# Kernel optimization log

Hardware: AMD Instinct MI355X
Metric: run time of the kernel (lower is better)

## Reference

```python
import jax, jax.numpy as jnp
import numpy as np

N0, N1 = 4096, 16384
HID, LAT, DIM, OUT = 128, 64, 3, 3
OFFS = [1, 2, 3, 5, 8]  # circulant graph offsets; A+A^3 support is offset sums


def _ring_edges(N, offs):
    # edge_index of A + A^3 for circulant adjacency with given offsets
    o = np.asarray(offs)
    s3 = (o[:, None, None] + o[None, :, None] + o[None, None, :]).ravel()
    aug = np.unique(np.concatenate([o, s3]))
    src = np.repeat(np.arange(N), aug.size)
    dst = (src + np.tile(aug, N)) % N
    return np.stack([src, dst]).astype(np.int32)


def _gatv2(x, src, dst, eattr, Wl, bl, Wr, br, We, att, bias, N):
    # PyG GATv2Conv, heads=1, add_self_loops=True with fill_value='mean'
    cnt = jax.ops.segment_sum(jnp.ones_like(dst, jnp.float32), dst, N)
    loop_attr = jax.ops.segment_sum(eattr, dst, N) / jnp.maximum(cnt, 1.0)[:, None]
    loops = jnp.arange(N, dtype=src.dtype)
    s = jnp.concatenate([src, loops])
    d = jnp.concatenate([dst, loops])
    ea = jnp.concatenate([eattr, loop_attr], 0)
    xl = x @ Wl.T + bl
    xr = x @ Wr.T + br
    m = xl[s] + xr[d] + ea @ We.T              # [E+N, HID]
    m = jnp.where(m > 0, m, 0.2 * m)           # leaky_relu(0.2)
    a = m @ att                                # [E+N]
    amax = jax.ops.segment_max(a, d, N)
    ex = jnp.exp(a - amax[d])
    den = jax.ops.segment_sum(ex, d, N)
    alpha = ex / (den[d] + 1e-16)
    return jax.ops.segment_sum(xl[s] * alpha[:, None], d, N) + bias


def _knn_interp(x, pos_x, pos_y, k=3):
    # PyG knn_interpolate: inverse-squared-distance weighted k-NN average
    d2 = (jnp.sum(pos_y ** 2, 1)[:, None] + jnp.sum(pos_x ** 2, 1)[None, :]
          - 2.0 * pos_y @ pos_x.T)             # [Ny, Nx]
    neg, idx = jax.lax.top_k(-d2, k)
    w = 1.0 / jnp.maximum(-neg, 1e-16)          # [Ny, k]
    return jnp.sum(x[idx] * w[..., None], 1) / jnp.sum(w, 1)[:, None]


def _forward(latent, pos0, pos1, eidx0, eidx1, conv_Wl, conv_bl, conv_Wr,
             conv_br, conv_We, conv_att, conv_bias, lin0_W, lin0_b, lins_W,
             lins_b, out_W, out_b):
    x = latent @ lin0_W.T + lin0_b
    src0, dst0 = eidx0[0], eidx0[1]
    ea0 = pos0[dst0] - pos0[src0]
    for c in (0, 1):
        h = jnp.concatenate([x, pos0], 1)
        x = jax.nn.elu(_gatv2(h, src0, dst0, ea0, conv_Wl[c], conv_bl[c],
                              conv_Wr[c], conv_br[c], conv_We[c], conv_att[c],
                              conv_bias[c], N0)) + h @ lins_W[c].T + lins_b[c]
    x = _knn_interp(x, pos0, pos1, 3)
    src1, dst1 = eidx1[0], eidx1[1]
    ea1 = pos1[dst1] - pos1[src1]
    for c in (2, 3):
        h = jnp.concatenate([x, pos1], 1)
        x = jax.nn.elu(_gatv2(h, src1, dst1, ea1, conv_Wl[c], conv_bl[c],
                              conv_Wr[c], conv_br[c], conv_We[c], conv_att[c],
                              conv_bias[c], N1)) + h @ lins_W[c].T + lins_b[c]
    h = jnp.concatenate([x, pos1], 1)
    return h @ out_W.T + out_b


def setup_inputs() -> dict:
    key = jax.random.key(0)
    ks = jax.random.split(key, 16)
    n = lambda i, shape, s=0.05: jax.random.normal(ks[i], shape, jnp.float32) * s
    IN = HID + DIM
    return dict(
        latent=jax.random.normal(ks[0], (N0, LAT), jnp.float32),
        pos0=jax.random.normal(ks[1], (N0, DIM), jnp.float32),
        pos1=jax.random.normal(ks[2], (N1, DIM), jnp.float32),
        eidx0=jnp.asarray(_ring_edges(N0, OFFS)),
        eidx1=jnp.asarray(_ring_edges(N1, OFFS)),
        conv_Wl=n(3, (4, HID, IN)), conv_bl=n(4, (4, HID)),
        conv_Wr=n(5, (4, HID, IN)), conv_br=n(6, (4, HID)),
        conv_We=n(7, (4, HID, DIM)), conv_att=n(8, (4, HID)),
        conv_bias=n(9, (4, HID)),
        lin0_W=n(10, (HID, LAT)), lin0_b=n(11, (HID,)),
        lins_W=n(12, (4, HID, IN)), lins_b=n(13, (4, HID)),
        out_W=n(14, (OUT, IN)), out_b=n(15, (OUT,)))


def reference(latent, pos0, pos1, eidx0, eidx1, conv_Wl, conv_bl, conv_Wr,
              conv_br, conv_We, conv_att, conv_bias, lin0_W, lin0_b, lins_W,
              lins_b, out_W, out_b):
    return _forward(latent, pos0, pos1, eidx0, eidx1, conv_Wl, conv_bl,
                    conv_Wr, conv_br, conv_We, conv_att, conv_bias, lin0_W,
                    lin0_b, lins_W, lins_b, out_W, out_b)
```

## Files before the change

### kernel.cpp

```cpp
#include <hip/hip_runtime.h>
#include <hip/hip_bf16.h>

#define N0 4096
#define N1 16384
#define HID 128
#define LAT 64
#define DIM 3
#define NAUG 21
#define JTOT 512
#define NG 5

typedef __attribute__((ext_vector_type(8))) short bf16x8;
typedef __attribute__((ext_vector_type(4))) float f32x4;

__device__ __constant__ int c_aug[NAUG] = {1,2,3,4,5,6,7,8,9,10,11,12,13,14,
                                           15,16,17,18,19,21,24};

__device__ __forceinline__ unsigned short f2bf(float v) {
    __hip_bfloat16 b = __float2bfloat16(v);
    return *reinterpret_cast<unsigned short*>(&b);
}

template<int CTRL>
__device__ __forceinline__ float dpp_xadd(float p) {
    return p + __int_as_float(__builtin_amdgcn_mov_dpp(
        __float_as_int(p), CTRL, 0xF, 0xF, true));
}

__device__ __forceinline__ float reduce32(float p) {
    p = dpp_xadd<0xB1>(p);
    p = dpp_xadd<0x4E>(p);
    p = dpp_xadd<0x128>(p);
    p += __shfl_xor(p, 4, 64);
    p += __shfl_xor(p, 16, 64);
    return p;
}

#define KCH 16
#define KCS 256
#define KNN_XPARTS 64
#define KNN_BLOCKS (KCH * KNN_XPARTS)

#define WSWZ_PER_LAYER 81920
#define H0G4 131072
#define H1G4 524288
#define P_NSWZ (4 * WSWZ_PER_LAYER)
#define P_B0 P_NSWZ
#define P_B1 (P_B0 + 4 * JTOT)
#define P_B2 (P_B1 + 64 * 128)
#define P_B3 (P_B2 + H0G4)
#define P_B4 (P_B3 + H1G4)
#define PREP_BLOCKS 3880

__global__ __launch_bounds__(256)
void prep_knn_kernel(const float* __restrict__ Wl,
                     const float* __restrict__ Wr,
                     const float* __restrict__ We,
                     const float* __restrict__ linsW,
                     const float* __restrict__ bl,
                     const float* __restrict__ br,
                     const float* __restrict__ linsb,
                     const float* __restrict__ lin0W,
                     const float* __restrict__ pos0,
                     const float* __restrict__ pos1,
                     unsigned short* __restrict__ Wswz,
                     float* __restrict__ bias_cat,
                     float* __restrict__ Wt0,
                     unsigned short* __restrict__ hswz0A,
                     unsigned short* __restrict__ hswz0B,
                     unsigned short* __restrict__ hswz1A,
                     unsigned short* __restrict__ hswz1B,
                     float* __restrict__ pb_d,
                     int* __restrict__ pb_i) {
    __shared__ float4 sx[KCS];

    if (blockIdx.x < KNN_BLOCKS) {
        int tid = threadIdx.x;
        int chunk = blockIdx.x >> 6;
        int xpart = blockIdx.x & 63;
        {
            const float* p = &pos0[(chunk * KCS + tid) * 3];
            float x = p[0], y = p[1], z = p[2];
            sx[tid] = make_float4(x, y, z, x * x + y * y + z * z);
        }
        __syncthreads();
        int y = xpart * 256 + tid;
        float p0 = pos1[y * 3], p1 = pos1[y * 3 + 1], p2 = pos1[y * 3 + 2];
        float m0 = -2.0f * p0, m1 = -2.0f * p1, m2 = -2.0f * p2;
        float sy = p0 * p0 + p1 * p1 + p2 * p2;
        float bd0 = 1e30f, bd1 = 1e30f, bd2 = 1e30f;
        int bi0 = 0, bi1 = 0, bi2 = 0;
        int gbase = chunk * KCS;
#pragma unroll 4
        for (int i = 0; i < KCS; i += 4) {
            float4 s[4];
#pragma unroll
            for (int v = 0; v < 4; ++v) s[v] = sx[i + v];
#pragma unroll
            for (int v = 0; v < 4; ++v) {
                int gi = gbase + i + v;
                float t = fmaf(m0, s[v].x, s[v].w);
                t = fmaf(m1, s[v].y, t);
                t = fmaf(m2, s[v].z, t);
                t += sy;
                bool c0 = t < bd0;
                bool c1 = t < bd1;
                bool c2 = t < bd2;
                float n0 = fminf(bd0, t);
                float n1 = __builtin_amdgcn_fmed3f(bd0, bd1, t);
                float n2 = __builtin_amdgcn_fmed3f(bd1, bd2, t);
                int j0 = c0 ? gi : bi0;
                int j1 = c0 ? bi0 : (c1 ? gi : bi1);
                int j2 = c1 ? bi1 : (c2 ? gi : bi2);
                bd0 = n0; bd1 = n1; bd2 = n2;
                bi0 = j0; bi1 = j1; bi2 = j2;
            }
        }
        int base = (chunk * N1 + y) * 3;
        pb_d[base] = bd0; pb_d[base + 1] = bd1; pb_d[base + 2] = bd2;
        pb_i[base] = bi0; pb_i[base + 1] = bi1; pb_i[base + 2] = bi2;
        return;
    }

    int tid = (blockIdx.x - KNN_BLOCKS) * blockDim.x + threadIdx.x;
    if (tid < P_NSWZ) {
        int c = tid / WSWZ_PER_LAYER;
        int r = tid - c * WSWZ_PER_LAYER;
        int nt = r / 2560;
        int g  = (r / 512) % 5;
        int l  = (r / 8) % 64;
        int j  = r % 8;
        int k  = g * 32 + (l >> 4) * 8 + j;
        int n  = nt * 16 + (l & 15);
        float v = 0.0f;
        if (k < 131) {
            if (n < 128)      v = Wl[(c * 128 + n) * 131 + k];
            else if (n < 256) v = Wr[(c * 128 + (n - 128)) * 131 + k];
            else if (n < 384) v = linsW[(c * 128 + (n - 256)) * 131 + k];
            else              v = (k >= 128) ? We[(c * 128 + (n - 384)) * 3 + (k - 128)]
                                             : 0.0f;
        }
        Wswz[tid] = f2bf(v);
    } else if (tid < P_B1) {
        int idx = tid - P_B0;
        int c = idx / JTOT;
        int j = idx - c * JTOT;
        float v;
        if (j < 128)        v = bl[c * 128 + j];
        else if (j < 256)   v = br[c * 128 + (j - 128)];
        else if (j < 384)   v = linsb[c * 128 + (j - 256)];
        else                v = 0.0f;
        bias_cat[idx] = v;
    } else if (tid < P_B2) {
        int idx = tid - P_B1;
        int k = idx / 128;
        int j = idx - k * 128;
        Wt0[idx] = lin0W[j * 64 + k];
    } else if (tid < P_B3) {
        int r = tid - P_B2;
        int j = r & 7;
        int l = (r >> 3) & 63;
        int mt = r >> 9;
        int row = mt * 16 + (l & 15);
        int k = 128 + (l >> 4) * 8 + j;
        float v = (k < 131) ? pos0[row * 3 + (k - 128)] : 0.0f;
        unsigned short bv = f2bf(v);
        size_t idx = (size_t)((mt * 5 + 4) * 64 + l) * 8 + j;
        hswz0A[idx] = bv;
        hswz0B[idx] = bv;
    } else if (tid < P_B4) {
        int r = tid - P_B3;
        int j = r & 7;
        int l = (r >> 3) & 63;
        int mt = r >> 9;
        int row = mt * 16 + (l & 15);
        int k = 128 + (l >> 4) * 8 + j;
        float v = (k < 131) ? pos1[row * 3 + (k - 128)] : 0.0f;
        unsigned short bv = f2bf(v);
        size_t idx = (size_t)((mt * 5 + 4) * 64 + l) * 8 + j;
        hswz1A[idx] = bv;
        hswz1B[idx] = bv;
    }
}

#define MERGE_BLOCKS 128

__global__ __launch_bounds__(128)
void lin0_merge_kernel(const float* __restrict__ latent,
                       const float* __restrict__ Wt0,
                       const float* __restrict__ b,
                       unsigned short* __restrict__ hswz0,
                       const float* __restrict__ pb_d,
                       const int* __restrict__ pb_i,
                       int* __restrict__ knn_idx,
                       float* __restrict__ knn_w) {
    __shared__ float lrow[64];

    if (blockIdx.x < MERGE_BLOCKS) {
        int y = blockIdx.x * 128 + threadIdx.x;
        float bd0 = 1e30f, bd1 = 1e30f, bd2 = 1e30f;
        int bi0 = 0, bi1 = 0, bi2 = 0;
        for (int c = 0; c < KCH; ++c) {
            int base = (c * N1 + y) * 3;
#pragma unroll
            for (int t3 = 0; t3 < 3; ++t3) {
                float t = pb_d[base + t3];
                int gi = pb_i[base + t3];
                bool c0 = t < bd0;
                bool c1 = t < bd1;
                bool c2 = t < bd2;
                float n0 = fminf(bd0, t);
                float n1 = __builtin_amdgcn_fmed3f(bd0, bd1, t);
                float n2 = __builtin_amdgcn_fmed3f(bd1, bd2, t);
                int j0 = c0 ? gi : bi0;
                int j1 = c0 ? bi0 : (c1 ? gi : bi1);
                int j2 = c1 ? bi1 : (c2 ? gi : bi2);
                bd0 = n0; bd1 = n1; bd2 = n2;
                bi0 = j0; bi1 = j1; bi2 = j2;
            }
        }
        knn_idx[y * 3]     = bi0;
        knn_idx[y * 3 + 1] = bi1;
        knn_idx[y * 3 + 2] = bi2;
        knn_w[y * 3]     = 1.0f / fmaxf(bd0, 1e-16f);
        knn_w[y * 3 + 1] = 1.0f / fmaxf(bd1, 1e-16f);
        knn_w[y * 3 + 2] = 1.0f / fmaxf(bd2, 1e-16f);
        return;
    }

    int n = blockIdx.x - MERGE_BLOCKS;
    int j = threadIdx.x;
    if (j < 64) lrow[j] = latent[n * 64 + j];
    __syncthreads();
    float acc = b[j];
#pragma unroll 8
    for (int k = 0; k < 64; ++k) acc += lrow[k] * Wt0[k * 128 + j];
    int g = j >> 5, sub = (j >> 3) & 3, jj = j & 7;
    hswz0[(size_t)(((n >> 4) * 5 + g) * 64 + sub * 16 + (n & 15)) * 8 + jj] = f2bf(acc);
}

#define WROW 40
#define FSTR 132

__device__ __forceinline__ void layer_body(
        const unsigned short* __restrict__ hswz,
        const unsigned short* __restrict__ Wswz,
        const float* __restrict__ bias_cat,
        const float* __restrict__ att,
        const float* __restrict__ bias,
        float* __restrict__ xout,
        unsigned short* __restrict__ hout,
        const float* __restrict__ outW,
        const float* __restrict__ outb,
        const float* __restrict__ pos1,
        int mode, int N, int mt0,
        float (*xls_s)[FSTR], float (*pes_s)[FSTR], float (*xr_s)[FSTR],
        float (*lin_s)[FSTR]) {
    int tid = threadIdx.x;
    int w = tid >> 6;
    int l = tid & 63;
    int quad = l >> 4, lcol = l & 15;
    int n0 = mt0 * 16;
    int MT = N >> 4;

    bf16x8 a[3][NG];
#pragma unroll
    for (int i = 0; i < 3; ++i) {
        int mt = mt0 - 2 + i;
        if (mt < 0) mt += MT;
#pragma unroll
        for (int g = 0; g < NG; ++g)
            a[i][g] = *(const bf16x8*)&hswz[(size_t)((mt * NG + g) * 64 + l) * 8];
    }

#pragma unroll
    for (int i = 0; i < 4; ++i) {
        int b = i * 8 + w;
        int colbase = (b & 7) * 16;
        int ntw, kind;
        if (b < 8)       { ntw = b;      kind = 0; }
        else if (b < 16) { ntw = 16 + b; kind = 1; }
        else if (b < 24) { ntw = b - 8;  kind = 2; }
        else             { ntw = b - 8;  kind = 3; }
        bf16x8 bf[NG];
#pragma unroll
        for (int g = 0; g < NG; ++g)
            bf[g] = *(const bf16x8*)&Wswz[(size_t)((ntw * NG + g) * 64 + l) * 8];
        float bv = bias_cat[ntw * 16 + lcol];
        if (kind < 2) {
            float (*dst)[FSTR] = (kind == 0) ? xls_s : pes_s;
#pragma unroll
            for (int m = 0; m < 3; ++m) {
                f32x4 c = {bv, bv, bv, bv};
#pragma unroll
                for (int g = 0; g < NG; ++g)
                    c = __builtin_amdgcn_mfma_f32_16x16x32_bf16(a[m][g], bf[g], c, 0, 0, 0);
                if (m == 0) {
                    if (quad >= 2) {
                        int w0 = (quad - 2) * 4;
#pragma unroll
                        for (int r = 0; r < 4; ++r) dst[w0 + r][colbase + lcol] = c[r];
                    }
                } else {
                    int w0 = m * 16 - 8 + quad * 4;
#pragma unroll
                    for (int r = 0; r < 4; ++r) dst[w0 + r][colbase + lcol] = c[r];
                }
            }
        } else {
            f32x4 c = {bv, bv, bv, bv};
#pragma unroll
            for (int g = 0; g < NG; ++g)
                c = __builtin_amdgcn_mfma_f32_16x16x32_bf16(a[2][g], bf[g], c, 0, 0, 0);
            float (*dst)[FSTR] = (kind == 2) ? xr_s : lin_s;
            int w0 = quad * 4;
#pragma unroll
            for (int r = 0; r < 4; ++r) dst[w0 + r][colbase + lcol] = c[r];
        }
    }
    __syncthreads();

    int qh = l >> 5;
    int t = l & 31;
    int dl = w * 2 + qh;
    int d = n0 + dl;
    int selfrow = dl + 24;
    int i0 = t * 4;

    f32x4 linv = *(const f32x4*)&lin_s[dl][i0];

    float att4[4], base[4], xld[4], pesum[4], o[4];
    {
        f32x4 a0 = *(const f32x4*)&att[i0];
        f32x4 r0 = *(const f32x4*)&xr_s[dl][i0];
        f32x4 x0 = *(const f32x4*)&xls_s[selfrow][i0];
        f32x4 p0 = *(const f32x4*)&pes_s[selfrow][i0];
#pragma unroll
        for (int j = 0; j < 4; ++j) {
            att4[j] = a0[j];
            xld[j]  = x0[j];
            base[j] = r0[j] + p0[j];
            pesum[j] = 0.0f;
            o[j] = 0.0f;
        }
    }

    float den = 0.0f;

#pragma unroll
    for (int k = 0; k < NAUG; ++k) {
        int lr = selfrow - c_aug[k];
        float xls[4], pes[4];
        *(f32x4*)&xls[0] = *(const f32x4*)&xls_s[lr][i0];
        *(f32x4*)&pes[0] = *(const f32x4*)&pes_s[lr][i0];
        float p = 0.0f;
#pragma unroll
        for (int j = 0; j < 4; ++j) {
            float mm = xls[j] + base[j] - pes[j];
            mm = mm > 0.0f ? mm : 0.2f * mm;
            p = fmaf(att4[j], mm, p);
            pesum[j] += pes[j];
        }
        p = reduce32(p);
        float wgt = __expf(p);
        den += wgt;
#pragma unroll
        for (int j = 0; j < 4; ++j) o[j] = fmaf(wgt, xls[j], o[j]);
    }
    {
        const float inv21 = 1.0f / 21.0f;
        float p = 0.0f;
#pragma unroll
        for (int j = 0; j < 4; ++j) {
            float mm = xld[j] + base[j] - pesum[j] * inv21;
            mm = mm > 0.0f ? mm : 0.2f * mm;
            p = fmaf(att4[j], mm, p);
        }
        p = reduce32(p);
        float wgt = __expf(p);
        den += wgt;
#pragma unroll
        for (int j = 0; j < 4; ++j) o[j] = fmaf(wgt, xld[j], o[j]);
    }

    float inv = 1.0f / (den + 1e-16f);
    float res[4];
    {
        f32x4 b0 = *(const f32x4*)&bias[i0];
#pragma unroll
        for (int j = 0; j < 4; ++j) {
            float v = o[j] * inv + b0[j];
            v = v > 0.0f ? v : __expf(v) - 1.0f;
            res[j] = v + linv[j];
        }
    }

    if (mode == 0) {
        *(f32x4*)&xout[(size_t)d * 128 + i0] = *(f32x4*)&res[0];
    } else if (mode == 1) {
        unsigned short ob[4];
#pragma unroll
        for (int j = 0; j < 4; ++j) ob[j] = f2bf(res[j]);
        int g = i0 >> 5, sub = (i0 >> 3) & 3, jj = i0 & 7;
        *(uint2*)&hout[(size_t)((((d >> 4) * 5 + g) * 64) + sub * 16 + (d & 15)) * 8 + jj]
            = *(uint2*)ob;
    } else {
        float po[3];
#pragma unroll
        for (int o3 = 0; o3 < 3; ++o3) {
            const float* wr = &outW[o3 * 131 + i0];
            float p = res[0] * wr[0];
            p = fmaf(res[1], wr[1], p);
            p = fmaf(res[2], wr[2], p);
            p = fmaf(res[3], wr[3], p);
            p = reduce32(p);
            po[o3] = p;
        }
        if (t == 0) {
            float p0 = pos1[d * 3], p1 = pos1[d * 3 + 1], p2 = pos1[d * 3 + 2];
#pragma unroll
            for (int o3 = 0; o3 < 3; ++o3) {
                xout[d * 3 + o3] = po[o3] + outb[o3] + p0 * outW[o3 * 131 + 128]
                                 + p1 * outW[o3 * 131 + 129] + p2 * outW[o3 * 131 + 130];
            }
        }
    }
}

__global__ __launch_bounds__(512, 2)
void fused_layer_kernel(const unsigned short* __restrict__ hswz,
                        const unsigned short* __restrict__ Wswz,
                        const float* __restrict__ bias_cat,
                        const float* __restrict__ att,
                        const float* __restrict__ bias,
                        float* __restrict__ xout,
                        unsigned short* __restrict__ hout,
                        const float* __restrict__ outW,
                        const float* __restrict__ outb,
                        const float* __restrict__ pos1,
                        int mode, int N) {
    __shared__ __align__(16) float xls_s[WROW][FSTR];
    __shared__ __align__(16) float pes_s[WROW][FSTR];
    __shared__ __align__(16) float xr_s[16][FSTR];
    __shared__ __align__(16) float lin_s[16][FSTR];
    layer_body(hswz, Wswz, bias_cat, att, bias, xout, hout,
               outW, outb, pos1, mode, N, blockIdx.x,
               xls_s, pes_s, xr_s, lin_s);
}

__global__ __launch_bounds__(256)
void interp_kernel(const float* __restrict__ x0, const int* __restrict__ knn_idx,
                   const float* __restrict__ knn_w, unsigned short* __restrict__ hswz) {
    int wave = threadIdx.x >> 6;
    int lane = threadIdx.x & 63;
    int y = blockIdx.x * 4 + wave;
    int i0 = 2 * lane;
    float w0 = knn_w[y * 3], w1 = knn_w[y * 3 + 1], w2 = knn_w[y * 3 + 2];
    int j0 = knn_idx[y * 3], j1 = knn_idx[y * 3 + 1], j2 = knn_idx[y * 3 + 2];
    float inv = 1.0f / (w0 + w1 + w2);
    float2 a = *(const float2*)&x0[(size_t)j0 * 128 + i0];
    float2 b = *(const float2*)&x0[(size_t)j1 * 128 + i0];
    float2 c = *(const float2*)&x0[(size_t)j2 * 128 + i0];
    float rx = (w0 * a.x + w1 * b.x + w2 * c.x) * inv;
    float ry = (w0 * a.y + w1 * b.y + w2 * c.y) * inv;
    unsigned int packed = (unsigned int)f2bf(rx) | ((unsigned int)f2bf(ry) << 16);
    int g = i0 >> 5, sub = (i0 >> 3) & 3, jj = i0 & 7;
    size_t idx = (size_t)((((y >> 4) * 5 + g) * 64) + sub * 16 + (y & 15)) * 8 + jj;
    *(unsigned int*)&hswz[idx] = packed;
}

extern "C" void kernel_launch(void* const* d_in, const int* in_sizes, int n_in,
                              void* d_out, int out_size, void* d_ws, size_t ws_size,
                              hipStream_t stream) {
    (void)in_sizes; (void)n_in; (void)out_size; (void)ws_size;
    const float* latent   = (const float*)d_in[0];
    const float* pos0     = (const float*)d_in[1];
    const float* pos1     = (const float*)d_in[2];
    const float* conv_Wl  = (const float*)d_in[5];
    const float* conv_bl  = (const float*)d_in[6];
    const float* conv_Wr  = (const float*)d_in[7];
    const float* conv_br  = (const float*)d_in[8];
    const float* conv_We  = (const float*)d_in[9];
    const float* conv_att = (const float*)d_in[10];
    const float* conv_bias= (const float*)d_in[11];
    const float* lin0_W   = (const float*)d_in[12];
    const float* lin0_b   = (const float*)d_in[13];
    const float* lins_W   = (const float*)d_in[14];
    const float* lins_b   = (const float*)d_in[15];
    const float* out_W    = (const float*)d_in[16];
    const float* out_b    = (const float*)d_in[17];
    float* out = (float*)d_out;

    char* ws = (char*)d_ws;
    unsigned short* Wswz = (unsigned short*)ws; ws += (size_t)4 * WSWZ_PER_LAYER * 2;
    float* bias_cat = (float*)ws;  ws += (size_t)4 * JTOT * 4;
    float* Wt0      = (float*)ws;  ws += (size_t)64 * 128 * 4;
    unsigned short* hswz0A = (unsigned short*)ws; ws += (size_t)(N0 / 16) * NG * 64 * 8 * 2;
    unsigned short* hswz0B = (unsigned short*)ws; ws += (size_t)(N0 / 16) * NG * 64 * 8 * 2;
    unsigned short* hswz1A = (unsigned short*)ws; ws += (size_t)(N1 / 16) * NG * 64 * 8 * 2;
    unsigned short* hswz1B = (unsigned short*)ws; ws += (size_t)(N1 / 16) * NG * 64 * 8 * 2;
    float* bufA     = (float*)ws;  ws += (size_t)N0 * 128 * 4;
    float* pb_d     = (float*)ws;  ws += (size_t)KCH * N1 * 3 * 4;
    int*   pb_i     = (int*)ws;    ws += (size_t)KCH * N1 * 3 * 4;
    int*   knn_idx  = (int*)ws;    ws += (size_t)N1 * 3 * 4;
    float* knn_w    = (float*)ws;  ws += (size_t)N1 * 3 * 4;

    prep_knn_kernel<<<KNN_BLOCKS + PREP_BLOCKS, 256, 0, stream>>>(
        conv_Wl, conv_Wr, conv_We, lins_W, conv_bl, conv_br, lins_b, lin0_W,
        pos0, pos1, Wswz, bias_cat, Wt0, hswz0A, hswz0B, hswz1A, hswz1B,
        pb_d, pb_i);

    lin0_merge_kernel<<<MERGE_BLOCKS + N0, 128, 0, stream>>>(
        latent, Wt0, lin0_b, hswz0A, pb_d, pb_i, knn_idx, knn_w);

    fused_layer_kernel<<<N0 / 16, 512, 0, stream>>>(
        hswz0A, Wswz + (size_t)0 * WSWZ_PER_LAYER, bias_cat + 0 * JTOT,
        conv_att + 0 * 128, conv_bias + 0 * 128, nullptr, hswz0B,
        nullptr, nullptr, nullptr, 1, N0);
    fused_layer_kernel<<<N0 / 16, 512, 0, stream>>>(
        hswz0B, Wswz + (size_t)1 * WSWZ_PER_LAYER, bias_cat + 1 * JTOT,
        conv_att + 1 * 128, conv_bias + 1 * 128, bufA, nullptr,
        nullptr, nullptr, nullptr, 0, N0);

    interp_kernel<<<N1 / 4, 256, 0, stream>>>(bufA, knn_idx, knn_w, hswz1A);

    fused_layer_kernel<<<N1 / 16, 512, 0, stream>>>(
        hswz1A, Wswz + (size_t)2 * WSWZ_PER_LAYER, bias_cat + 2 * JTOT,
        conv_att + 2 * 128, conv_bias + 2 * 128, nullptr, hswz1B,
        nullptr, nullptr, nullptr, 1, N1);
    fused_layer_kernel<<<N1 / 16, 512, 0, stream>>>(
        hswz1B, Wswz + (size_t)3 * WSWZ_PER_LAYER, bias_cat + 3 * JTOT,
        conv_att + 3 * 128, conv_bias + 3 * 128, out, nullptr,
        out_W, out_b, pos1, 2, N1);
}
```

Before: 203.1 us.

## Fuse kNN interpolation into first fine-level GAT layer kernel

Removes the separate interp kernel and its global hswz1A buffer. Each fine-level layer block now computes the interpolated features, plus the pos columns for its 3 halo tiles, straight into shared memory and reads its A fragments from there. This drops one launch and one global round trip, but each tile's interpolation is recomputed three times across neighbouring blocks. The change also replaces one shuffle-xor step in the reduction with a DPP row-shift add.

```diff
diff --git a/kernel.cpp b/kernel.cpp
--- a/kernel.cpp
+++ b/kernel.cpp
@@ -31,7 +31,7 @@
     p = dpp_xadd<0xB1>(p);
     p = dpp_xadd<0x4E>(p);
     p = dpp_xadd<0x128>(p);
-    p += __shfl_xor(p, 4, 64);
+    p = dpp_xadd<0x124>(p);
     p += __shfl_xor(p, 16, 64);
     return p;
 }
@@ -68,7 +68,6 @@
                      float* __restrict__ Wt0,
                      unsigned short* __restrict__ hswz0A,
                      unsigned short* __restrict__ hswz0B,
-                     unsigned short* __restrict__ hswz1A,
                      unsigned short* __restrict__ hswz1B,
                      float* __restrict__ pb_d,
                      int* __restrict__ pb_i) {
@@ -176,10 +175,7 @@
         int row = mt * 16 + (l & 15);
         int k = 128 + (l >> 4) * 8 + j;
         float v = (k < 131) ? pos1[row * 3 + (k - 128)] : 0.0f;
-        unsigned short bv = f2bf(v);
-        size_t idx = (size_t)((mt * 5 + 4) * 64 + l) * 8 + j;
-        hswz1A[idx] = bv;
-        hswz1B[idx] = bv;
+        hswz1B[(size_t)((mt * 5 + 4) * 64 + l) * 8 + j] = f2bf(v);
     }
 }
 
@@ -244,6 +240,7 @@
 
 __device__ __forceinline__ void layer_body(
         const unsigned short* __restrict__ hswz,
+        const unsigned short* hloc,
         const unsigned short* __restrict__ Wswz,
         const float* __restrict__ bias_cat,
         const float* __restrict__ att,
@@ -264,13 +261,22 @@
     int MT = N >> 4;
 
     bf16x8 a[3][NG];
-#pragma unroll
-    for (int i = 0; i < 3; ++i) {
-        int mt = mt0 - 2 + i;
-        if (mt < 0) mt += MT;
-#pragma unroll
-        for (int g = 0; g < NG; ++g)
-            a[i][g] = *(const bf16x8*)&hswz[(size_t)((mt * NG + g) * 64 + l) * 8];
+    if (hloc) {
+#pragma unroll
+        for (int i = 0; i < 3; ++i)
+#pragma unroll
+            for (int g = 0; g < NG; ++g)
+                a[i][g] = *(const bf16x8*)&hloc[(size_t)(((i * NG + g) * 64) + l) * 8];
+        __syncthreads();
+    } else {
+#pragma unroll
+        for (int i = 0; i < 3; ++i) {
+            int mt = mt0 - 2 + i;
+            if (mt < 0) mt += MT;
+#pragma unroll
+            for (int g = 0; g < NG; ++g)
+                a[i][g] = *(const bf16x8*)&hswz[(size_t)((mt * NG + g) * 64 + l) * 8];
+        }
     }
 
 #pragma unroll
@@ -443,30 +449,64 @@
     __shared__ __align__(16) float pes_s[WROW][FSTR];
     __shared__ __align__(16) float xr_s[16][FSTR];
     __shared__ __align__(16) float lin_s[16][FSTR];
-    layer_body(hswz, Wswz, bias_cat, att, bias, xout, hout,
+    layer_body(hswz, nullptr, Wswz, bias_cat, att, bias, xout, hout,
                outW, outb, pos1, mode, N, blockIdx.x,
                xls_s, pes_s, xr_s, lin_s);
 }
 
-__global__ __launch_bounds__(256)
-void interp_kernel(const float* __restrict__ x0, const int* __restrict__ knn_idx,
-                   const float* __restrict__ knn_w, unsigned short* __restrict__ hswz) {
-    int wave = threadIdx.x >> 6;
-    int lane = threadIdx.x & 63;
-    int y = blockIdx.x * 4 + wave;
-    int i0 = 2 * lane;
-    float w0 = knn_w[y * 3], w1 = knn_w[y * 3 + 1], w2 = knn_w[y * 3 + 2];
-    int j0 = knn_idx[y * 3], j1 = knn_idx[y * 3 + 1], j2 = knn_idx[y * 3 + 2];
-    float inv = 1.0f / (w0 + w1 + w2);
-    float2 a = *(const float2*)&x0[(size_t)j0 * 128 + i0];
-    float2 b = *(const float2*)&x0[(size_t)j1 * 128 + i0];
-    float2 c = *(const float2*)&x0[(size_t)j2 * 128 + i0];
-    float rx = (w0 * a.x + w1 * b.x + w2 * c.x) * inv;
-    float ry = (w0 * a.y + w1 * b.y + w2 * c.y) * inv;
-    unsigned int packed = (unsigned int)f2bf(rx) | ((unsigned int)f2bf(ry) << 16);
-    int g = i0 >> 5, sub = (i0 >> 3) & 3, jj = i0 & 7;
-    size_t idx = (size_t)((((y >> 4) * 5 + g) * 64) + sub * 16 + (y & 15)) * 8 + jj;
-    *(unsigned int*)&hswz[idx] = packed;
+__global__ __launch_bounds__(512, 2)
+void fused_layer2_kernel(const float* __restrict__ bufA,
+                         const int* __restrict__ knn_idx,
+                         const float* __restrict__ knn_w,
+                         const float* __restrict__ pos1,
+                         const unsigned short* __restrict__ Wswz,
+                         const float* __restrict__ bias_cat,
+                         const float* __restrict__ att,
+                         const float* __restrict__ bias,
+                         unsigned short* __restrict__ hout) {
+    __shared__ __align__(16) float xls_s[WROW][FSTR];
+    __shared__ __align__(16) float pes_s[WROW][FSTR];
+    __shared__ __align__(16) float xr_s[16][FSTR];
+    __shared__ __align__(16) float lin_s[16][FSTR];
+
+    unsigned short* hloc = (unsigned short*)&xls_s[0][0];
+    int tid = threadIdx.x;
+    int mt0 = blockIdx.x;
+    int MT = N1 >> 4;
+
+    for (int item = tid; item < 3 * NG * 64 * 4; item += 512) {
+        int jp = item & 3;
+        int l  = (item >> 2) & 63;
+        int gq = item >> 8;
+        int g  = gq % NG;
+        int i  = gq / NG;
+        int mt = mt0 - 2 + i;
+        if (mt < 0) mt += MT;
+        int y  = mt * 16 + (l & 15);
+        int col = g * 32 + ((l >> 4) << 3) + 2 * jp;
+        unsigned int packed;
+        if (col < 128) {
+            float w0 = knn_w[y * 3], w1 = knn_w[y * 3 + 1], w2 = knn_w[y * 3 + 2];
+            int j0 = knn_idx[y * 3], j1 = knn_idx[y * 3 + 1], j2 = knn_idx[y * 3 + 2];
+            float inv = 1.0f / (w0 + w1 + w2);
+            float2 a = *(const float2*)&bufA[(size_t)j0 * 128 + col];
+            float2 b = *(const float2*)&bufA[(size_t)j1 * 128 + col];
+            float2 c = *(const float2*)&bufA[(size_t)j2 * 128 + col];
+            float rx = (w0 * a.x + w1 * b.x + w2 * c.x) * inv;
+            float ry = (w0 * a.y + w1 * b.y + w2 * c.y) * inv;
+            packed = (unsigned int)f2bf(rx) | ((unsigned int)f2bf(ry) << 16);
+        } else {
+            float v0 = (col < 131) ? pos1[y * 3 + (col - 128)] : 0.0f;
+            float v1 = (col + 1 < 131) ? pos1[y * 3 + (col - 127)] : 0.0f;
+            packed = (unsigned int)f2bf(v0) | ((unsigned int)f2bf(v1) << 16);
+        }
+        *(unsigned int*)&hloc[(size_t)item * 2] = packed;
+    }
+    __syncthreads();
+
+    layer_body(nullptr, hloc, Wswz, bias_cat, att, bias, nullptr, hout,
+               nullptr, nullptr, nullptr, 1, N1, mt0,
+               xls_s, pes_s, xr_s, lin_s);
 }
 
 extern "C" void kernel_launch(void* const* d_in, const int* in_sizes, int n_in,
@@ -497,7 +537,6 @@
     float* Wt0      = (float*)ws;  ws += (size_t)64 * 128 * 4;
     unsigned short* hswz0A = (unsigned short*)ws; ws += (size_t)(N0 / 16) * NG * 64 * 8 * 2;
     unsigned short* hswz0B = (unsigned short*)ws; ws += (size_t)(N0 / 16) * NG * 64 * 8 * 2;
-    unsigned short* hswz1A = (unsigned short*)ws; ws += (size_t)(N1 / 16) * NG * 64 * 8 * 2;
     unsigned short* hswz1B = (unsigned short*)ws; ws += (size_t)(N1 / 16) * NG * 64 * 8 * 2;
     float* bufA     = (float*)ws;  ws += (size_t)N0 * 128 * 4;
     float* pb_d     = (float*)ws;  ws += (size_t)KCH * N1 * 3 * 4;
@@ -507,7 +546,7 @@
 
     prep_knn_kernel<<<KNN_BLOCKS + PREP_BLOCKS, 256, 0, stream>>>(
         conv_Wl, conv_Wr, conv_We, lins_W, conv_bl, conv_br, lins_b, lin0_W,
-        pos0, pos1, Wswz, bias_cat, Wt0, hswz0A, hswz0B, hswz1A, hswz1B,
+        pos0, pos1, Wswz, bias_cat, Wt0, hswz0A, hswz0B, hswz1B,
         pb_d, pb_i);
 
     lin0_merge_kernel<<<MERGE_BLOCKS + N0, 128, 0, stream>>>(
@@ -522,12 +561,11 @@
         conv_att + 1 * 128, conv_bias + 1 * 128, bufA, nullptr,
         nullptr, nullptr, nullptr, 0, N0);
 
-    interp_kernel<<<N1 / 4, 256, 0, stream>>>(bufA, knn_idx, knn_w, hswz1A);
-
-    fused_layer_kernel<<<N1 / 16, 512, 0, stream>>>(
-        hswz1A, Wswz + (size_t)2 * WSWZ_PER_LAYER, bias_cat + 2 * JTOT,
-        conv_att + 2 * 128, conv_bias + 2 * 128, nullptr, hswz1B,
-        nullptr, nullptr, nullptr, 1, N1);
+    fused_layer2_kernel<<<N1 / 16, 512, 0, stream>>>(
+        bufA, knn_idx, knn_w, pos1,
+        Wswz + (size_t)2 * WSWZ_PER_LAYER, bias_cat + 2 * JTOT,
+        conv_att + 2 * 128, conv_bias + 2 * 128, hswz1B);
+
     fused_layer_kernel<<<N1 / 16, 512, 0, stream>>>(
         hswz1B, Wswz + (size_t)3 * WSWZ_PER_LAYER, bias_cat + 3 * JTOT,
         conv_att + 3 * 128, conv_bias + 3 * 128, out, nullptr,
```

Result: slower. 211.2 us (+4.0%).
